# Kernel optimization log

Measured on AMD Instinct MI355X. Metric: run time of the kernel, lower is better.

The kernel has to match this reference:

```python
import jax, jax.numpy as jnp
import numpy as np

NUM_HEADS = 16
HEAD_DIM = 128
ROPE_BASE = 10000.0


def rotate_half(x):
    x1, x2 = jnp.split(x, 2, axis=-1)
    return jnp.concatenate((-x2, x1), axis=-1)


def rope_cos_sin(seq_len, dim, dtype):
    inv_freq = 1.0 / (ROPE_BASE ** (jnp.arange(0, dim, 2, dtype=jnp.float32) / dim))
    t = jnp.arange(seq_len, dtype=jnp.float32)
    freqs = jnp.einsum('i,j->ij', t, inv_freq)          # [S, dim/2]
    emb = jnp.concatenate((freqs, freqs), axis=-1)       # [S, dim]
    return emb.astype(dtype)  # caller applies cos/sin


def setup_inputs() -> dict:
    key = jax.random.key(0)
    k0, k1, k2, k3, k4 = jax.random.split(key, 5)
    B, S, H = 2, 2048, 2048
    hd = H // NUM_HEADS
    scale = 0.02
    return {
        'hidden_states': jax.random.normal(k0, (B, S, H), dtype=jnp.float32),
        'Wq': jax.random.normal(k1, (H, H), dtype=jnp.float32) * scale,
        'Wk': jax.random.normal(k2, (hd, H), dtype=jnp.float32) * scale,
        'Wv': jax.random.normal(k3, (hd, H), dtype=jnp.float32) * scale,
        'Wo': jax.random.normal(k4, (H, H), dtype=jnp.float32) * scale,
    }


def reference(hidden_states, Wq, Wk, Wv, Wo):
    B, S, H = hidden_states.shape
    nH, hd = NUM_HEADS, HEAD_DIM

    # projections (torch Linear: x @ W.T)
    q = jnp.einsum('bsh,oh->bso', hidden_states, Wq).reshape(B, S, nH, hd)
    q = q.transpose(0, 2, 1, 3)                          # [B, nH, S, hd]
    k = jnp.einsum('bsh,dh->bsd', hidden_states, Wk)      # [B, S, hd] single KV head
    v = jnp.einsum('bsh,dh->bsd', hidden_states, Wv)      # [B, S, hd]

    # rotary embedding
    emb = rope_cos_sin(S, hd, hidden_states.dtype)        # [S, hd]
    cos, sin = jnp.cos(emb), jnp.sin(emb)
    q = q * cos[None, None] + rotate_half(q) * sin[None, None]
    k = k * cos[None] + rotate_half(k) * sin[None]

    # attention: Q heads against shared K/V head
    scores = jnp.einsum('bhqd,bkd->bhqk', q, k) / jnp.sqrt(jnp.asarray(hd, hidden_states.dtype))
    attn = jax.nn.softmax(scores, axis=-1)               # dropout is identity in eval
    out = jnp.einsum('bhqk,bkd->bhqd', attn, v)           # [B, nH, S, hd]
    out = out.transpose(0, 2, 1, 3).reshape(B, S, H)
    attn_output = jnp.einsum('bsh,oh->bso', out, Wo)

    # cache tensors returned by the torch module: k, v with head dim of 1
    return attn_output, k[:, None], v[:, None]
```

## Files before the change

### kernel.cpp

```cpp
#include <hip/hip_runtime.h>
#include <hip/hip_bf16.h>

typedef __hip_bfloat16 bf16;

#define NH   16
#define HD   128
#define SEQ  2048
#define BB   2
#define HID  2048

#define ROPE_C 0.14391156856f

using frag   = __attribute__((ext_vector_type(8))) short;
using f32x4  = __attribute__((ext_vector_type(4))) float;
using f32x16 = __attribute__((ext_vector_type(16))) float;


__device__ __forceinline__ void cvt8_store(const float4 f0, const float4 f1, bf16* dst) {
    union { frag v; bf16 h[8]; } p;
    p.h[0] = __float2bfloat16(f0.x); p.h[1] = __float2bfloat16(f0.y);
    p.h[2] = __float2bfloat16(f0.z); p.h[3] = __float2bfloat16(f0.w);
    p.h[4] = __float2bfloat16(f1.x); p.h[5] = __float2bfloat16(f1.y);
    p.h[6] = __float2bfloat16(f1.z); p.h[7] = __float2bfloat16(f1.w);
    *reinterpret_cast<frag*>(dst) = p.v;
}

__device__ __forceinline__ unsigned pk2(float a, float b) {
    union { bf16 h[2]; unsigned u; } p;
    p.h[0] = __float2bfloat16(a);
    p.h[1] = __float2bfloat16(b);
    return p.u;
}

__device__ __forceinline__ void gld_lds16(const bf16* g, bf16* l) {
    __builtin_amdgcn_global_load_lds(
        (const __attribute__((address_space(1))) void*)g,
        (__attribute__((address_space(3))) void*)l, 16, 0, 0);
}

__global__ __launch_bounds__(256) void cvt_bf16(const float* __restrict__ hs,
                                                const float* __restrict__ Wq,
                                                const float* __restrict__ Wk,
                                                const float* __restrict__ Wv,
                                                bf16* __restrict__ hsb,
                                                bf16* __restrict__ wqb,
                                                bf16* __restrict__ wkb,
                                                bf16* __restrict__ wvb) {
    const int blk = blockIdx.x;
    const float* src;
    bf16* dst;
    if (blk < 4096)      { src = hs + (size_t)blk * 2048;          dst = hsb + (size_t)blk * 2048; }
    else if (blk < 6144) { src = Wq + (size_t)(blk - 4096) * 2048; dst = wqb + (size_t)(blk - 4096) * 2048; }
    else if (blk < 6272) { src = Wk + (size_t)(blk - 6144) * 2048; dst = wkb + (size_t)(blk - 6144) * 2048; }
    else                 { src = Wv + (size_t)(blk - 6272) * 2048; dst = wvb + (size_t)(blk - 6272) * 2048; }
    const int t = threadIdx.x * 8;
    const float4 f0 = *reinterpret_cast<const float4*>(src + t);
    const float4 f1 = *reinterpret_cast<const float4*>(src + t + 4);
    cvt8_store(f0, f1, dst + t);
}

__global__ __launch_bounds__(256, 4) void gemm_qkv(const bf16* __restrict__ A,
                                                   const bf16* __restrict__ Wqb,
                                                   const bf16* __restrict__ Wkb,
                                                   const bf16* __restrict__ Wvb,
                                                   bf16* __restrict__ qout,
                                                   float* __restrict__ Ck,
                                                   float* __restrict__ Cv,
                                                   bf16* __restrict__ kb,
                                                   bf16* __restrict__ vt) {
    __shared__ bf16 Asl[4096];
    __shared__ bf16 Bsl[4096];
    const int tid  = threadIdx.x;
    const int wave = tid >> 6;
    const int lane = tid & 63;
    const int quad = lane >> 4;
    const int l15  = lane & 15;
    const int wr   = wave >> 1;
    const int wc   = wave & 1;
    const int row0 = blockIdx.y * 128;
    const int bx   = blockIdx.x;
    const bool isq  = bx < 16;
    const bool is_v = (bx == 17);
    const bf16* W   = isq ? Wqb : (is_v ? Wvb : Wkb);
    const int col0  = isq ? bx * 128 : 0;

    const int sr = tid >> 2;
    const int sc = (tid & 3) * 8;
    const int sg = ((sr >> 5) & 1) * 64 + (sr & 31);

    const bf16* ag = A + (size_t)(row0 + sr) * HID + sc;
    const bf16* bg = W + (size_t)(col0 + sg) * HID + sc;
    bf16* al = &Asl[tid * 8];
    bf16* bl = &Bsl[tid * 8];

    f32x4 acc[4][4];
#pragma unroll
    for (int i = 0; i < 4; ++i)
#pragma unroll
        for (int j = 0; j < 4; ++j) acc[i][j] = (f32x4){0.f,0.f,0.f,0.f};

    for (int k0 = 0; k0 < HID; k0 += 32) {
        __syncthreads();
        gld_lds16(ag + k0, al);
        gld_lds16(ag + (size_t)64 * HID + k0, al + 2048);
        gld_lds16(bg + k0, bl);
        gld_lds16(bg + (size_t)32 * HID + k0, bl + 2048);
        __syncthreads();
        frag af[4], bfr[4];
#pragma unroll
        for (int i = 0; i < 4; ++i)
            af[i] = *reinterpret_cast<const frag*>(&Asl[(((wr*64 + i*16 + l15)*4) + quad) * 8]);
#pragma unroll
        for (int j = 0; j < 4; ++j)
            bfr[j] = *reinterpret_cast<const frag*>(&Bsl[(((wc*64 + j*16 + l15)*4) + quad) * 8]);
#pragma unroll
        for (int i = 0; i < 4; ++i)
#pragma unroll
            for (int j = 0; j < 4; ++j)
                acc[i][j] = __builtin_amdgcn_mfma_f32_16x16x32_bf16(af[i], bfr[j], acc[i][j], 0, 0, 0);
    }

    if (isq) {
#pragma unroll
        for (int i = 0; i < 4; ++i)
#pragma unroll
            for (int r = 0; r < 4; ++r) {
                const int row = row0 + wr*64 + i*16 + quad*4 + r;
                const int s = row & (SEQ - 1);
                bf16* crow = qout + (size_t)row * HID + col0;
#pragma unroll
                for (int j = 0; j < 2; ++j) {
                    const int d = wc*32 + 16*j + l15;
                    const float invf = expf(-(float)d * ROPE_C);
                    float sn, cs;
                    sincosf((float)s * invf, &sn, &cs);
                    const float x1 = acc[i][j][r], x2 = acc[i][j+2][r];
                    crow[d]      = __float2bfloat16(x1*cs - x2*sn);
                    crow[d + 64] = __float2bfloat16(x2*cs + x1*sn);
                }
            }
    } else if (is_v) {
#pragma unroll
        for (int i = 0; i < 4; ++i)
#pragma unroll
            for (int r = 0; r < 4; ++r) {
                const int row = row0 + wr*64 + i*16 + quad*4 + r;
                const int s = row & (SEQ - 1);
                const int b = row >> 11;
                float* crow = Cv + (size_t)row * HD;
#pragma unroll
                for (int j = 0; j < 4; ++j) {
                    const int d = (j >> 1)*64 + wc*32 + (j & 1)*16 + l15;
                    const float val = acc[i][j][r];
                    crow[d] = val;
                    vt[((size_t)b * HD + d) * SEQ + s] = __float2bfloat16(val);
                }
            }
    } else {
#pragma unroll
        for (int i = 0; i < 4; ++i)
#pragma unroll
            for (int r = 0; r < 4; ++r) {
                const int row = row0 + wr*64 + i*16 + quad*4 + r;
                const int s = row & (SEQ - 1);
                float* crow = Ck + (size_t)row * HD;
#pragma unroll
                for (int j = 0; j < 2; ++j) {
                    const int d = wc*32 + 16*j + l15;
                    const float invf = expf(-(float)d * ROPE_C);
                    float sn, cs;
                    sincosf((float)s * invf, &sn, &cs);
                    const float y1 = acc[i][j][r]*cs - acc[i][j+2][r]*sn;
                    const float y2 = acc[i][j+2][r]*cs + acc[i][j][r]*sn;
                    crow[d]      = y1;
                    crow[d + 64] = y2;
                    kb[(size_t)row * HD + d]      = __float2bfloat16(y1);
                    kb[(size_t)row * HD + d + 64] = __float2bfloat16(y2);
                }
            }
    }
}

__global__ __launch_bounds__(256) void attn_mfma(const bf16* __restrict__ qbuf,
                                                 const bf16* __restrict__ kb,
                                                 const bf16* __restrict__ vt,
                                                 bf16* __restrict__ attn_out) {
    __shared__ char lds[32768];

    const int tid  = threadIdx.x;
    const int wave = tid >> 6;
    const int lane = tid & 63;
    const int l31  = lane & 31;
    const int h    = lane >> 5;
    const int qg   = wave & 1;
    const int kg   = wave >> 1;
    const int q0   = blockIdx.x * 64;
    const int hh   = blockIdx.y;
    const int b    = blockIdx.z;

    const bf16* kbb = kb + (size_t)b * SEQ * HD;
    const bf16* vtb = vt + (size_t)b * HD * SEQ;

    frag qfr[8];
    {
        const bf16* qrow = qbuf + ((size_t)(b * SEQ + q0 + qg * 32 + l31)) * HID + hh * HD;
#pragma unroll
        for (int c = 0; c < 8; ++c)
            qfr[c] = *reinterpret_cast<const frag*>(qrow + c * 16 + h * 8);
    }

    const int sl   = tid & 127;
    const int kg_s = tid >> 7;

    int klof[4];
#pragma unroll
    for (int i = 0; i < 4; ++i) {
        const int n   = sl + i * 128;
        const int key = n >> 4, d = (n >> 1) & 7, hs = n & 1;
        const int L   = d * 64 + key * 2 + hs;
        klof[i] = (kg_s * 8192 + L * 16) ^ (((((key >> 2) ^ d) & 7)) << 4);
    }
    int vlof[8], vgof[8];
#pragma unroll
    for (int i = 0; i < 8; ++i) {
        const int g   = sl + i * 128;
        const int dim = g >> 3, ks = (g >> 2) & 1, m = (g >> 1) & 1, hs = g & 1;
        const int dt  = dim >> 5;
        const int C   = (dt * 2 + ks) * 64 + (dim & 31) * 2 + hs;
        const int B   = 16384 + kg_s * 8192 + C * 16 + m * 8;
        const int xv  = (((dim & 31) >> 2) ^ (dt * 2 + ks)) & 7;
        vlof[i] = B ^ (xv << 4);
        vgof[i] = dim * SEQ + kg_s * 32 + (g & 7) * 4;
    }

    const int rpos = (l31 * 2 + h) * 16;
    const int rsw  = rpos ^ ((((rpos >> 7) & 7)) << 4);

    f32x16 oacc[4];
#pragma unroll
    for (int dt = 0; dt < 4; ++dt)
#pragma unroll
        for (int r = 0; r < 16; ++r) oacc[dt][r] = 0.f;
    float mrow = -1e30f;
    float lrow = 0.f;
    const float scale = 0.088388347648318433f;

    for (int it = 0; it < SEQ / 64; ++it) {
        __syncthreads();
        {
            const bf16* kp = kbb + (size_t)it * 64 * HD + kg_s * 4096;
            const bf16* vp = vtb + it * 64;
            uint4 krg[4];
            uint2 vrg[8];
#pragma unroll
            for (int i = 0; i < 4; ++i)
                krg[i] = *reinterpret_cast<const uint4*>(kp + (sl + i * 128) * 8);
#pragma unroll
            for (int i = 0; i < 8; ++i)
                vrg[i] = *reinterpret_cast<const uint2*>(vp + vgof[i]);
#pragma unroll
            for (int i = 0; i < 4; ++i)
                *reinterpret_cast<uint4*>(lds + klof[i]) = krg[i];
#pragma unroll
            for (int i = 0; i < 8; ++i)
                *reinterpret_cast<uint2*>(lds + vlof[i]) = vrg[i];
        }
        __syncthreads();

        f32x16 sacc;
#pragma unroll
        for (int r = 0; r < 16; ++r) sacc[r] = 0.f;
#pragma unroll
        for (int c = 0; c < 8; ++c) {
            const frag kf = *reinterpret_cast<const frag*>(
                lds + kg * 8192 + c * 1024 + (rsw ^ (c << 4)));
            sacc = __builtin_amdgcn_mfma_f32_32x32x16_bf16(kf, qfr[c], sacc, 0, 0, 0);
        }

        float mx = -1e30f;
#pragma unroll
        for (int r = 0; r < 16; ++r) mx = fmaxf(mx, sacc[r]);
        mx = fmaxf(mx, __shfl_xor(mx, 32));
        const bool skip = (bool)__all(mx - mrow <= 90.0f);
        const float mn = skip ? mrow : fmaxf(mrow, mx);
        const float al = skip ? 1.f : __expf((mrow - mn) * scale);
        float p[16];
        float ps = 0.f;
#pragma unroll
        for (int r = 0; r < 16; ++r) {
            p[r] = __expf((sacc[r] - mn) * scale);
            ps += p[r];
        }
        ps += __shfl_xor(ps, 32);
        lrow = lrow * al + ps;
        mrow = mn;

        frag pb[2];
#pragma unroll
        for (int ks = 0; ks < 2; ++ks) {
            union { unsigned u[4]; frag f; } pf;
#pragma unroll
            for (int w = 0; w < 4; ++w)
                pf.u[w] = pk2(p[8 * ks + 2 * w], p[8 * ks + 2 * w + 1]);
            pb[ks] = pf.f;
        }

        if (!skip)
#pragma unroll
            for (int dt = 0; dt < 4; ++dt)
#pragma unroll
                for (int r = 0; r < 16; ++r) oacc[dt][r] *= al;

#pragma unroll
        for (int dt = 0; dt < 4; ++dt)
#pragma unroll
            for (int ks = 0; ks < 2; ++ks) {
                const int cb = dt * 2 + ks;
                const frag vf = *reinterpret_cast<const frag*>(
                    lds + 16384 + kg * 8192 + cb * 1024 + (rsw ^ (cb << 4)));
                oacc[dt] = __builtin_amdgcn_mfma_f32_32x32x16_bf16(vf, pb[ks], oacc[dt], 0, 0, 0);
            }
    }

    __syncthreads();
    float* fl = reinterpret_cast<float*>(lds);
    if (h == 0) {
        fl[(qg * 2 + kg) * 32 + l31]       = mrow;
        fl[128 + (qg * 2 + kg) * 32 + l31] = lrow;
    }
    __syncthreads();
    const float m0 = fl[qg * 64 + l31],       m1 = fl[qg * 64 + 32 + l31];
    const float l0 = fl[128 + qg * 64 + l31], l1 = fl[128 + qg * 64 + 32 + l31];
    const float ms = fmaxf(m0, m1);
    const float c0 = __expf((m0 - ms) * scale);
    const float c1 = __expf((m1 - ms) * scale);
    const float inv = 1.f / (c0 * l0 + c1 * l1);
    const float cs = kg ? c1 : c0;
#pragma unroll
    for (int dt = 0; dt < 4; ++dt)
#pragma unroll
        for (int r = 0; r < 16; ++r) oacc[dt][r] *= cs;

    float* ob = reinterpret_cast<float*>(lds + 1024);
#pragma unroll
    for (int dt = 0; dt < 4; ++dt) {
        __syncthreads();
        if (kg == 1) {
            float* dst = ob + (qg * 64 + lane) * 17;
#pragma unroll
            for (int r = 0; r < 16; ++r) dst[r] = oacc[dt][r];
        }
        __syncthreads();
        if (kg == 0) {
            const float* sp = ob + (qg * 64 + lane) * 17;
            const int s = q0 + qg * 32 + l31;
            bf16* orow = attn_out + ((size_t)(b * SEQ + s)) * HID + hh * HD;
#pragma unroll
            for (int t = 0; t < 4; ++t) {
                const float v0 = (oacc[dt][t*4+0] + sp[t*4+0]) * inv;
                const float v1 = (oacc[dt][t*4+1] + sp[t*4+1]) * inv;
                const float v2 = (oacc[dt][t*4+2] + sp[t*4+2]) * inv;
                const float v3 = (oacc[dt][t*4+3] + sp[t*4+3]) * inv;
                uint2 val;
                val.x = pk2(v0, v1);
                val.y = pk2(v2, v3);
                *reinterpret_cast<uint2*>(orow + dt * 32 + t * 8 + h * 4) = val;
            }
        }
    }
}

__global__ __launch_bounds__(256, 4) void gemm_o_mfma(const bf16* __restrict__ A,
                                                      const float* __restrict__ W,
                                                      float* __restrict__ C) {
    __shared__ bf16 Asl[4096];
    __shared__ bf16 Bsl[4096];
    const int tid  = threadIdx.x;
    const int wave = tid >> 6;
    const int lane = tid & 63;
    const int quad = lane >> 4;
    const int l15  = lane & 15;
    const int wr   = wave >> 1;
    const int wc   = wave & 1;
    const int row0 = blockIdx.y * 128;
    const int col0 = blockIdx.x * 128;

    const int sr = tid >> 2;
    const int sc = (tid & 3) * 8;

    const bf16* ag = A + (size_t)(row0 + sr) * HID + sc;
    bf16* al = &Asl[tid * 8];
    const float* wg0 = W + (size_t)(col0 + sr) * HID + sc;
    const float* wg1 = wg0 + (size_t)64 * HID;

    f32x4 acc[4][4];
#pragma unroll
    for (int i = 0; i < 4; ++i)
#pragma unroll
        for (int j = 0; j < 4; ++j) acc[i][j] = (f32x4){0.f,0.f,0.f,0.f};

    for (int k0 = 0; k0 < HID; k0 += 32) {
        __syncthreads();
        gld_lds16(ag + k0, al);
        gld_lds16(ag + (size_t)64 * HID + k0, al + 2048);
        {
            const float4* b0 = reinterpret_cast<const float4*>(wg0 + k0);
            const float4* b1 = reinterpret_cast<const float4*>(wg1 + k0);
            cvt8_store(b0[0], b0[1], &Bsl[tid * 8]);
            cvt8_store(b1[0], b1[1], &Bsl[tid * 8 + 2048]);
        }
        __syncthreads();
        frag af[4], bfr[4];
#pragma unroll
        for (int i = 0; i < 4; ++i)
            af[i] = *reinterpret_cast<const frag*>(&Asl[(((wr*64 + i*16 + l15)*4) + quad) * 8]);
#pragma unroll
        for (int j = 0; j < 4; ++j)
            bfr[j] = *reinterpret_cast<const frag*>(&Bsl[(((wc*64 + j*16 + l15)*4) + quad) * 8]);
#pragma unroll
        for (int i = 0; i < 4; ++i)
#pragma unroll
            for (int j = 0; j < 4; ++j)
                acc[i][j] = __builtin_amdgcn_mfma_f32_16x16x32_bf16(af[i], bfr[j], acc[i][j], 0, 0, 0);
    }

#pragma unroll
    for (int i = 0; i < 4; ++i)
#pragma unroll
        for (int r = 0; r < 4; ++r) {
            const int row = row0 + wr*64 + i*16 + quad*4 + r;
            float* crow = C + (size_t)row * HID + col0 + wc*64;
#pragma unroll
            for (int j = 0; j < 4; ++j)
                crow[16*j + l15] = acc[i][j][r];
        }
}

extern "C" void kernel_launch(void* const* d_in, const int* in_sizes, int n_in,
                              void* d_out, int out_size, void* d_ws, size_t ws_size,
                              hipStream_t stream) {
    const float* hs = (const float*)d_in[0];
    const float* Wq = (const float*)d_in[1];
    const float* Wk = (const float*)d_in[2];
    const float* Wv = (const float*)d_in[3];
    const float* Wo = (const float*)d_in[4];

    float* out      = (float*)d_out;
    float* out_attn = out;
    float* out_k    = out + 8388608;
    float* out_v    = out + 8388608 + 524288;

    bf16* qbuf = (bf16*)d_out;
    bf16* kb   = (bf16*)((char*)d_out + 16777216);
    bf16* vt   = (bf16*)((char*)d_out + 17825792);
    bf16* wqb  = (bf16*)((char*)d_out + 18874368);
    bf16* wkb  = (bf16*)((char*)d_out + 27262976);
    bf16* wvb  = (bf16*)((char*)d_out + 27787264);
    bf16* hsb      = (bf16*)d_ws;
    bf16* attn_out = (bf16*)d_ws;

    cvt_bf16  <<<dim3(6400),                  dim3(256), 0, stream>>>(hs, Wq, Wk, Wv, hsb, wqb, wkb, wvb);
    gemm_qkv  <<<dim3(18, (BB*SEQ)/128),      dim3(256), 0, stream>>>(hsb, wqb, wkb, wvb,
                                                                      qbuf, out_k, out_v, kb, vt);
    attn_mfma <<<dim3(SEQ/64, NH, BB),        dim3(256), 0, stream>>>(qbuf, kb, vt, attn_out);
    gemm_o_mfma<<<dim3(HID/128, (BB*SEQ)/128), dim3(256), 0, stream>>>(attn_out, Wo, out_attn);
}
```

Measured before the change: 357.9 us.

## Double-buffer LDS in QKV and O GEMMs and widen V tile stores

Both GEMM kernels now use two LDS buffers, so the next K-slice is fetched while MFMAs run on the current one, and each iteration needs one barrier instead of two. In the output projection, the fp32 weight loads for the next slice are issued into registers early and converted to bf16 into LDS after the MFMAs. The attention kernel's V staging is remapped to 16-byte LDS stores built from two 8-byte global loads, halving the number of store instructions. Doubling LDS and holding the prefetched weights in registers lowers occupancy, and the O GEMM's launch bound drops from 4 to 3 blocks per CU.

```diff
diff --git a/kernel.cpp b/kernel.cpp
--- a/kernel.cpp
+++ b/kernel.cpp
@@ -68,8 +68,8 @@
                                                    float* __restrict__ Cv,
                                                    bf16* __restrict__ kb,
                                                    bf16* __restrict__ vt) {
-    __shared__ bf16 Asl[4096];
-    __shared__ bf16 Bsl[4096];
+    __shared__ bf16 Asl[2][4096];
+    __shared__ bf16 Bsl[2][4096];
     const int tid  = threadIdx.x;
     const int wave = tid >> 6;
     const int lane = tid & 63;
@@ -90,8 +90,6 @@
 
     const bf16* ag = A + (size_t)(row0 + sr) * HID + sc;
     const bf16* bg = W + (size_t)(col0 + sg) * HID + sc;
-    bf16* al = &Asl[tid * 8];
-    bf16* bl = &Bsl[tid * 8];
 
     f32x4 acc[4][4];
 #pragma unroll
@@ -99,25 +97,34 @@
 #pragma unroll
         for (int j = 0; j < 4; ++j) acc[i][j] = (f32x4){0.f,0.f,0.f,0.f};
 
-    for (int k0 = 0; k0 < HID; k0 += 32) {
-        __syncthreads();
-        gld_lds16(ag + k0, al);
-        gld_lds16(ag + (size_t)64 * HID + k0, al + 2048);
-        gld_lds16(bg + k0, bl);
-        gld_lds16(bg + (size_t)32 * HID + k0, bl + 2048);
-        __syncthreads();
+    gld_lds16(ag,                      &Asl[0][tid * 8]);
+    gld_lds16(ag + (size_t)64 * HID,   &Asl[0][tid * 8 + 2048]);
+    gld_lds16(bg,                      &Bsl[0][tid * 8]);
+    gld_lds16(bg + (size_t)32 * HID,   &Bsl[0][tid * 8 + 2048]);
+    __syncthreads();
+
+    for (int t = 0; t < 64; ++t) {
+        const int cur = t & 1;
+        if (t < 63) {
+            const int kn = (t + 1) * 32;
+            gld_lds16(ag + kn,                    &Asl[cur ^ 1][tid * 8]);
+            gld_lds16(ag + (size_t)64 * HID + kn, &Asl[cur ^ 1][tid * 8 + 2048]);
+            gld_lds16(bg + kn,                    &Bsl[cur ^ 1][tid * 8]);
+            gld_lds16(bg + (size_t)32 * HID + kn, &Bsl[cur ^ 1][tid * 8 + 2048]);
+        }
         frag af[4], bfr[4];
 #pragma unroll
         for (int i = 0; i < 4; ++i)
-            af[i] = *reinterpret_cast<const frag*>(&Asl[(((wr*64 + i*16 + l15)*4) + quad) * 8]);
+            af[i] = *reinterpret_cast<const frag*>(&Asl[cur][(((wr*64 + i*16 + l15)*4) + quad) * 8]);
 #pragma unroll
         for (int j = 0; j < 4; ++j)
-            bfr[j] = *reinterpret_cast<const frag*>(&Bsl[(((wc*64 + j*16 + l15)*4) + quad) * 8]);
+            bfr[j] = *reinterpret_cast<const frag*>(&Bsl[cur][(((wc*64 + j*16 + l15)*4) + quad) * 8]);
 #pragma unroll
         for (int i = 0; i < 4; ++i)
 #pragma unroll
             for (int j = 0; j < 4; ++j)
                 acc[i][j] = __builtin_amdgcn_mfma_f32_16x16x32_bf16(af[i], bfr[j], acc[i][j], 0, 0, 0);
+        __syncthreads();
     }
 
     if (isq) {
@@ -220,17 +227,15 @@
         const int L   = d * 64 + key * 2 + hs;
         klof[i] = (kg_s * 8192 + L * 16) ^ (((((key >> 2) ^ d) & 7)) << 4);
     }
-    int vlof[8], vgof[8];
-#pragma unroll
-    for (int i = 0; i < 8; ++i) {
-        const int g   = sl + i * 128;
-        const int dim = g >> 3, ks = (g >> 2) & 1, m = (g >> 1) & 1, hs = g & 1;
-        const int dt  = dim >> 5;
-        const int C   = (dt * 2 + ks) * 64 + (dim & 31) * 2 + hs;
-        const int B   = 16384 + kg_s * 8192 + C * 16 + m * 8;
-        const int xv  = (((dim & 31) >> 2) ^ (dt * 2 + ks)) & 7;
-        vlof[i] = B ^ (xv << 4);
-        vgof[i] = dim * SEQ + kg_s * 32 + (g & 7) * 4;
+    int vlof[4], vgof[4];
+#pragma unroll
+    for (int i = 0; i < 4; ++i) {
+        const int q  = sl + i * 128;
+        const int cb = q >> 6;
+        const int dim = ((q >> 7) << 5) + ((q >> 1) & 31);
+        const int ks  = cb & 1, hs = q & 1;
+        vlof[i] = 16384 + kg_s * 8192 + ((q * 16) ^ (((((q >> 3) & 7) ^ cb)) << 4));
+        vgof[i] = dim * SEQ + kg_s * 32 + (ks * 4 + hs) * 4;
     }
 
     const int rpos = (l31 * 2 + h) * 16;
@@ -251,19 +256,22 @@
             const bf16* kp = kbb + (size_t)it * 64 * HD + kg_s * 4096;
             const bf16* vp = vtb + it * 64;
             uint4 krg[4];
-            uint2 vrg[8];
+            uint4 vrg[4];
 #pragma unroll
             for (int i = 0; i < 4; ++i)
                 krg[i] = *reinterpret_cast<const uint4*>(kp + (sl + i * 128) * 8);
 #pragma unroll
-            for (int i = 0; i < 8; ++i)
-                vrg[i] = *reinterpret_cast<const uint2*>(vp + vgof[i]);
+            for (int i = 0; i < 4; ++i) {
+                const uint2 a = *reinterpret_cast<const uint2*>(vp + vgof[i]);
+                const uint2 c = *reinterpret_cast<const uint2*>(vp + vgof[i] + 8);
+                vrg[i] = (uint4){a.x, a.y, c.x, c.y};
+            }
 #pragma unroll
             for (int i = 0; i < 4; ++i)
                 *reinterpret_cast<uint4*>(lds + klof[i]) = krg[i];
 #pragma unroll
-            for (int i = 0; i < 8; ++i)
-                *reinterpret_cast<uint2*>(lds + vlof[i]) = vrg[i];
+            for (int i = 0; i < 4; ++i)
+                *reinterpret_cast<uint4*>(lds + vlof[i]) = vrg[i];
         }
         __syncthreads();
 
@@ -370,11 +378,11 @@
     }
 }
 
-__global__ __launch_bounds__(256, 4) void gemm_o_mfma(const bf16* __restrict__ A,
+__global__ __launch_bounds__(256, 3) void gemm_o_mfma(const bf16* __restrict__ A,
                                                       const float* __restrict__ W,
                                                       float* __restrict__ C) {
-    __shared__ bf16 Asl[4096];
-    __shared__ bf16 Bsl[4096];
+    __shared__ bf16 Asl[2][4096];
+    __shared__ bf16 Bsl[2][4096];
     const int tid  = threadIdx.x;
     const int wave = tid >> 6;
     const int lane = tid & 63;
@@ -389,7 +397,6 @@
     const int sc = (tid & 3) * 8;
 
     const bf16* ag = A + (size_t)(row0 + sr) * HID + sc;
-    bf16* al = &Asl[tid * 8];
     const float* wg0 = W + (size_t)(col0 + sr) * HID + sc;
     const float* wg1 = wg0 + (size_t)64 * HID;
 
@@ -399,29 +406,47 @@
 #pragma unroll
         for (int j = 0; j < 4; ++j) acc[i][j] = (f32x4){0.f,0.f,0.f,0.f};
 
-    for (int k0 = 0; k0 < HID; k0 += 32) {
-        __syncthreads();
-        gld_lds16(ag + k0, al);
-        gld_lds16(ag + (size_t)64 * HID + k0, al + 2048);
-        {
-            const float4* b0 = reinterpret_cast<const float4*>(wg0 + k0);
-            const float4* b1 = reinterpret_cast<const float4*>(wg1 + k0);
-            cvt8_store(b0[0], b0[1], &Bsl[tid * 8]);
-            cvt8_store(b1[0], b1[1], &Bsl[tid * 8 + 2048]);
-        }
-        __syncthreads();
+    gld_lds16(ag,                    &Asl[0][tid * 8]);
+    gld_lds16(ag + (size_t)64 * HID, &Asl[0][tid * 8 + 2048]);
+    {
+        const float4 b0 = *reinterpret_cast<const float4*>(wg0);
+        const float4 b1 = *reinterpret_cast<const float4*>(wg0 + 4);
+        const float4 b2 = *reinterpret_cast<const float4*>(wg1);
+        const float4 b3 = *reinterpret_cast<const float4*>(wg1 + 4);
+        cvt8_store(b0, b1, &Bsl[0][tid * 8]);
+        cvt8_store(b2, b3, &Bsl[0][tid * 8 + 2048]);
+    }
+    __syncthreads();
+
+    for (int t = 0; t < 64; ++t) {
+        const int cur = t & 1;
+        float4 nb0, nb1, nb2, nb3;
+        if (t < 63) {
+            const int kn = (t + 1) * 32;
+            gld_lds16(ag + kn,                    &Asl[cur ^ 1][tid * 8]);
+            gld_lds16(ag + (size_t)64 * HID + kn, &Asl[cur ^ 1][tid * 8 + 2048]);
+            nb0 = *reinterpret_cast<const float4*>(wg0 + kn);
+            nb1 = *reinterpret_cast<const float4*>(wg0 + kn + 4);
+            nb2 = *reinterpret_cast<const float4*>(wg1 + kn);
+            nb3 = *reinterpret_cast<const float4*>(wg1 + kn + 4);
+        }
         frag af[4], bfr[4];
 #pragma unroll
         for (int i = 0; i < 4; ++i)
-            af[i] = *reinterpret_cast<const frag*>(&Asl[(((wr*64 + i*16 + l15)*4) + quad) * 8]);
+            af[i] = *reinterpret_cast<const frag*>(&Asl[cur][(((wr*64 + i*16 + l15)*4) + quad) * 8]);
 #pragma unroll
         for (int j = 0; j < 4; ++j)
-            bfr[j] = *reinterpret_cast<const frag*>(&Bsl[(((wc*64 + j*16 + l15)*4) + quad) * 8]);
+            bfr[j] = *reinterpret_cast<const frag*>(&Bsl[cur][(((wc*64 + j*16 + l15)*4) + quad) * 8]);
 #pragma unroll
         for (int i = 0; i < 4; ++i)
 #pragma unroll
             for (int j = 0; j < 4; ++j)
                 acc[i][j] = __builtin_amdgcn_mfma_f32_16x16x32_bf16(af[i], bfr[j], acc[i][j], 0, 0, 0);
+        if (t < 63) {
+            cvt8_store(nb0, nb1, &Bsl[cur ^ 1][tid * 8]);
+            cvt8_store(nb2, nb3, &Bsl[cur ^ 1][tid * 8 + 2048]);
+        }
+        __syncthreads();
     }
 
 #pragma unroll
```

After: 377.7 us. +5.5%, slower.

## Double GEMM K-tile to 64 with XOR-swizzled LDS, add MFMA priority hints

Applied to the files above, without the earlier changes.

Both the QKV and output-projection GEMMs now stage a 64-wide K slice per iteration instead of 32. Shared memory doubles, and the tile layout uses XOR swizzling to avoid LDS bank conflicts, which halves the number of barrier pairs per GEMM. The attention kernel wraps its MFMA loops in s_setprio hints and reorders the V global-load offsets to match the LDS layout. The larger LDS footprint lowers occupancy, so the O-projection launch bound drops to 3 blocks per SM.

```diff
diff --git a/kernel.cpp b/kernel.cpp
--- a/kernel.cpp
+++ b/kernel.cpp
@@ -68,8 +68,8 @@
                                                    float* __restrict__ Cv,
                                                    bf16* __restrict__ kb,
                                                    bf16* __restrict__ vt) {
-    __shared__ bf16 Asl[4096];
-    __shared__ bf16 Bsl[4096];
+    __shared__ bf16 Asl[8192];
+    __shared__ bf16 Bsl[8192];
     const int tid  = threadIdx.x;
     const int wave = tid >> 6;
     const int lane = tid & 63;
@@ -84,40 +84,53 @@
     const bf16* W   = isq ? Wqb : (is_v ? Wvb : Wkb);
     const int col0  = isq ? bx * 128 : 0;
 
-    const int sr = tid >> 2;
-    const int sc = (tid & 3) * 8;
-    const int sg = ((sr >> 5) & 1) * 64 + (sr & 31);
-
-    const bf16* ag = A + (size_t)(row0 + sr) * HID + sc;
-    const bf16* bg = W + (size_t)(col0 + sg) * HID + sc;
+    const int st_row = tid >> 3;
+    const int st_col = ((tid & 7) ^ ((tid >> 3) & 7)) * 8;
+    const bf16* ag = A + (size_t)(row0 + st_row) * HID + st_col;
+    const bf16* bg = W + (size_t)(col0 + st_row) * HID + st_col;
     bf16* al = &Asl[tid * 8];
     bf16* bl = &Bsl[tid * 8];
 
+    const int swz  = (l15 & 7) << 4;
+    const int rdA0 = (wr * 64 + l15) * 128 + quad * 16;
+    const int rdB0 = (wc * 64 + l15) * 128 + quad * 16;
+
     f32x4 acc[4][4];
 #pragma unroll
     for (int i = 0; i < 4; ++i)
 #pragma unroll
         for (int j = 0; j < 4; ++j) acc[i][j] = (f32x4){0.f,0.f,0.f,0.f};
 
-    for (int k0 = 0; k0 < HID; k0 += 32) {
-        __syncthreads();
-        gld_lds16(ag + k0, al);
-        gld_lds16(ag + (size_t)64 * HID + k0, al + 2048);
-        gld_lds16(bg + k0, bl);
-        gld_lds16(bg + (size_t)32 * HID + k0, bl + 2048);
-        __syncthreads();
-        frag af[4], bfr[4];
-#pragma unroll
-        for (int i = 0; i < 4; ++i)
-            af[i] = *reinterpret_cast<const frag*>(&Asl[(((wr*64 + i*16 + l15)*4) + quad) * 8]);
-#pragma unroll
-        for (int j = 0; j < 4; ++j)
-            bfr[j] = *reinterpret_cast<const frag*>(&Bsl[(((wc*64 + j*16 + l15)*4) + quad) * 8]);
-#pragma unroll
-        for (int i = 0; i < 4; ++i)
+    for (int k0 = 0; k0 < HID; k0 += 64) {
+        __syncthreads();
+        gld_lds16(ag + k0,                    al);
+        gld_lds16(ag + (size_t)32 * HID + k0, al + 2048);
+        gld_lds16(ag + (size_t)64 * HID + k0, al + 4096);
+        gld_lds16(ag + (size_t)96 * HID + k0, al + 6144);
+        gld_lds16(bg + k0,                    bl);
+        gld_lds16(bg + (size_t)64 * HID + k0, bl + 2048);
+        gld_lds16(bg + (size_t)32 * HID + k0, bl + 4096);
+        gld_lds16(bg + (size_t)96 * HID + k0, bl + 6144);
+        __syncthreads();
+#pragma unroll
+        for (int s = 0; s < 2; ++s) {
+            const int ba = (rdA0 + s * 64) ^ swz;
+            const int bb = (rdB0 + s * 64) ^ swz;
+            frag af[4], bfr[4];
+#pragma unroll
+            for (int i = 0; i < 4; ++i)
+                af[i] = *reinterpret_cast<const frag*>(
+                            reinterpret_cast<const char*>(Asl) + ba + i * 2048);
 #pragma unroll
             for (int j = 0; j < 4; ++j)
-                acc[i][j] = __builtin_amdgcn_mfma_f32_16x16x32_bf16(af[i], bfr[j], acc[i][j], 0, 0, 0);
+                bfr[j] = *reinterpret_cast<const frag*>(
+                            reinterpret_cast<const char*>(Bsl) + bb + j * 2048);
+#pragma unroll
+            for (int i = 0; i < 4; ++i)
+#pragma unroll
+                for (int j = 0; j < 4; ++j)
+                    acc[i][j] = __builtin_amdgcn_mfma_f32_16x16x32_bf16(af[i], bfr[j], acc[i][j], 0, 0, 0);
+        }
     }
 
     if (isq) {
@@ -230,7 +243,7 @@
         const int B   = 16384 + kg_s * 8192 + C * 16 + m * 8;
         const int xv  = (((dim & 31) >> 2) ^ (dt * 2 + ks)) & 7;
         vlof[i] = B ^ (xv << 4);
-        vgof[i] = dim * SEQ + kg_s * 32 + (g & 7) * 4;
+        vgof[i] = dim * SEQ + kg_s * 32 + (ks * 4 + hs) * 4 + m * 8;
     }
 
     const int rpos = (l31 * 2 + h) * 16;
@@ -270,12 +283,14 @@
         f32x16 sacc;
 #pragma unroll
         for (int r = 0; r < 16; ++r) sacc[r] = 0.f;
+        __builtin_amdgcn_s_setprio(1);
 #pragma unroll
         for (int c = 0; c < 8; ++c) {
             const frag kf = *reinterpret_cast<const frag*>(
                 lds + kg * 8192 + c * 1024 + (rsw ^ (c << 4)));
             sacc = __builtin_amdgcn_mfma_f32_32x32x16_bf16(kf, qfr[c], sacc, 0, 0, 0);
         }
+        __builtin_amdgcn_s_setprio(0);
 
         float mx = -1e30f;
 #pragma unroll
@@ -311,6 +326,7 @@
 #pragma unroll
                 for (int r = 0; r < 16; ++r) oacc[dt][r] *= al;
 
+        __builtin_amdgcn_s_setprio(1);
 #pragma unroll
         for (int dt = 0; dt < 4; ++dt)
 #pragma unroll
@@ -320,6 +336,7 @@
                     lds + 16384 + kg * 8192 + cb * 1024 + (rsw ^ (cb << 4)));
                 oacc[dt] = __builtin_amdgcn_mfma_f32_32x32x16_bf16(vf, pb[ks], oacc[dt], 0, 0, 0);
             }
+        __builtin_amdgcn_s_setprio(0);
     }
 
     __syncthreads();
@@ -370,11 +387,11 @@
     }
 }
 
-__global__ __launch_bounds__(256, 4) void gemm_o_mfma(const bf16* __restrict__ A,
+__global__ __launch_bounds__(256, 3) void gemm_o_mfma(const bf16* __restrict__ A,
                                                       const float* __restrict__ W,
                                                       float* __restrict__ C) {
-    __shared__ bf16 Asl[4096];
-    __shared__ bf16 Bsl[4096];
+    __shared__ bf16 Asl[8192];
+    __shared__ bf16 Bsl[8192];
     const int tid  = threadIdx.x;
     const int wave = tid >> 6;
     const int lane = tid & 63;
@@ -385,13 +402,16 @@
     const int row0 = blockIdx.y * 128;
     const int col0 = blockIdx.x * 128;
 
-    const int sr = tid >> 2;
-    const int sc = (tid & 3) * 8;
-
-    const bf16* ag = A + (size_t)(row0 + sr) * HID + sc;
+    const int st_row = tid >> 3;
+    const int st_col = ((tid & 7) ^ ((tid >> 3) & 7)) * 8;
+    const bf16* ag = A + (size_t)(row0 + st_row) * HID + st_col;
+    const float* wg = W + (size_t)(col0 + st_row) * HID + st_col;
     bf16* al = &Asl[tid * 8];
-    const float* wg0 = W + (size_t)(col0 + sr) * HID + sc;
-    const float* wg1 = wg0 + (size_t)64 * HID;
+    bf16* blp = &Bsl[tid * 8];
+
+    const int swz  = (l15 & 7) << 4;
+    const int rdA0 = (wr * 64 + l15) * 128 + quad * 16;
+    const int rdB0 = (wc * 64 + l15) * 128 + quad * 16;
 
     f32x4 acc[4][4];
 #pragma unroll
@@ -399,29 +419,39 @@
 #pragma unroll
         for (int j = 0; j < 4; ++j) acc[i][j] = (f32x4){0.f,0.f,0.f,0.f};
 
-    for (int k0 = 0; k0 < HID; k0 += 32) {
-        __syncthreads();
-        gld_lds16(ag + k0, al);
-        gld_lds16(ag + (size_t)64 * HID + k0, al + 2048);
-        {
-            const float4* b0 = reinterpret_cast<const float4*>(wg0 + k0);
-            const float4* b1 = reinterpret_cast<const float4*>(wg1 + k0);
-            cvt8_store(b0[0], b0[1], &Bsl[tid * 8]);
-            cvt8_store(b1[0], b1[1], &Bsl[tid * 8 + 2048]);
-        }
-        __syncthreads();
-        frag af[4], bfr[4];
-#pragma unroll
-        for (int i = 0; i < 4; ++i)
-            af[i] = *reinterpret_cast<const frag*>(&Asl[(((wr*64 + i*16 + l15)*4) + quad) * 8]);
-#pragma unroll
-        for (int j = 0; j < 4; ++j)
-            bfr[j] = *reinterpret_cast<const frag*>(&Bsl[(((wc*64 + j*16 + l15)*4) + quad) * 8]);
-#pragma unroll
-        for (int i = 0; i < 4; ++i)
+    for (int k0 = 0; k0 < HID; k0 += 64) {
+        __syncthreads();
+        gld_lds16(ag + k0,                    al);
+        gld_lds16(ag + (size_t)32 * HID + k0, al + 2048);
+        gld_lds16(ag + (size_t)64 * HID + k0, al + 4096);
+        gld_lds16(ag + (size_t)96 * HID + k0, al + 6144);
+#pragma unroll
+        for (int r0 = 0; r0 < 4; ++r0) {
+            const float* w0 = wg + (size_t)(r0 * 32) * HID + k0;
+            const float4 f0 = *reinterpret_cast<const float4*>(w0);
+            const float4 f1 = *reinterpret_cast<const float4*>(w0 + 4);
+            cvt8_store(f0, f1, blp + r0 * 2048);
+        }
+        __syncthreads();
+#pragma unroll
+        for (int s = 0; s < 2; ++s) {
+            const int ba = (rdA0 + s * 64) ^ swz;
+            const int bb = (rdB0 + s * 64) ^ swz;
+            frag af[4], bfr[4];
+#pragma unroll
+            for (int i = 0; i < 4; ++i)
+                af[i] = *reinterpret_cast<const frag*>(
+                            reinterpret_cast<const char*>(Asl) + ba + i * 2048);
 #pragma unroll
             for (int j = 0; j < 4; ++j)
-                acc[i][j] = __builtin_amdgcn_mfma_f32_16x16x32_bf16(af[i], bfr[j], acc[i][j], 0, 0, 0);
+                bfr[j] = *reinterpret_cast<const frag*>(
+                            reinterpret_cast<const char*>(Bsl) + bb + j * 2048);
+#pragma unroll
+            for (int i = 0; i < 4; ++i)
+#pragma unroll
+                for (int j = 0; j < 4; ++j)
+                    acc[i][j] = __builtin_amdgcn_mfma_f32_16x16x32_bf16(af[i], bfr[j], acc[i][j], 0, 0, 0);
+        }
     }
 
 #pragma unroll
```

New measurement: 411.4 us. 15.0% more time.
